# Optimization experiments

Measured on AMD Instinct MI355X. Metric: run time of the kernel, lower is better.

The kernel has to match this reference:

```python
import jax, jax.numpy as jnp
import numpy as np

LEAKY_SLOPE = 0.2

def gcn_conv(x, W, b, src, dst, deg_inv_sqrt, num_nodes):
    # GCNConv: out = D^{-1/2} (A+I) D^{-1/2} X W + b
    h = x @ W                                   # [N, out]
    norm = deg_inv_sqrt[src] * deg_inv_sqrt[dst]  # [E']
    msg = h[src] * norm[:, None]                # gather + scale
    out = jax.ops.segment_sum(msg, dst, num_segments=num_nodes)
    return out + b

def gcn_forward(x, edge_index, W1, b1, W2, b2, W3, b3):
    num_nodes = x.shape[0]
    loop = jnp.arange(num_nodes, dtype=edge_index.dtype)
    src = jnp.concatenate([edge_index[0], loop])  # add self-loops
    dst = jnp.concatenate([edge_index[1], loop])
    deg = jax.ops.segment_sum(jnp.ones_like(dst, dtype=x.dtype), dst,
                              num_segments=num_nodes)
    deg_inv_sqrt = jnp.where(deg > 0, jax.lax.rsqrt(deg), 0.0)
    # dropout is identity in eval mode (training=False)
    h = gcn_conv(x, W1, b1, src, dst, deg_inv_sqrt, num_nodes)
    h = jax.nn.leaky_relu(h, negative_slope=LEAKY_SLOPE)
    h = gcn_conv(h, W2, b2, src, dst, deg_inv_sqrt, num_nodes)
    h = jax.nn.leaky_relu(h, negative_slope=LEAKY_SLOPE)
    h = gcn_conv(h, W3, b3, src, dst, deg_inv_sqrt, num_nodes)
    return h

def setup_inputs() -> dict:
    key = jax.random.key(0)
    ks = jax.random.split(key, 8)
    N, F, E, C = 100000, 256, 3200000, 40
    x = jax.random.normal(ks[0], (N, F), dtype=jnp.float32)
    edge_index = jax.random.randint(ks[1], (2, E), 0, N, dtype=jnp.int64)
    W1 = jax.random.normal(ks[2], (F, 128), dtype=jnp.float32) * (1.0 / np.sqrt(F))
    b1 = jnp.zeros((128,), dtype=jnp.float32)
    W2 = jax.random.normal(ks[3], (128, 16), dtype=jnp.float32) * (1.0 / np.sqrt(128))
    b2 = jnp.zeros((16,), dtype=jnp.float32)
    W3 = jax.random.normal(ks[4], (16, C), dtype=jnp.float32) * (1.0 / np.sqrt(16))
    b3 = jnp.zeros((C,), dtype=jnp.float32)
    return {"x": x, "edge_index": edge_index, "W1": W1, "b1": b1,
            "W2": W2, "b2": b2, "W3": W3, "b3": b3}

def reference(x, edge_index, W1, b1, W2, b2, W3, b3):
    return gcn_forward(x, edge_index, W1, b1, W2, b2, W3, b3)
```

## Files before the change

kernel.cpp:

```cpp
#include <hip/hip_runtime.h>
#include <hip/hip_fp16.h>
#include <math.h>

#define LEAKY 0.2f
#define BP 6
#define BSZ 64
#define NBUK_MAX 2048

typedef _Float16 f16x8 __attribute__((ext_vector_type(8)));
typedef _Float16 f16x2 __attribute__((ext_vector_type(2)));
typedef float f32x4 __attribute__((ext_vector_type(4)));

union H2 { __half2 h; f16x2 f; int i; };
union H8 { __half2 h[4]; float4 f; };
union H4 { __half2 h[2]; float2 f; };

__device__ inline __half2 shfl_xor_h2(__half2 v, int m) {
    H2 u; u.h = v;
    u.i = __shfl_xor(u.i, m);
    return u.h;
}

__global__ __launch_bounds__(256) void kinit(const int* __restrict__ dst,
                                             int* __restrict__ bhist,
                                             int* __restrict__ bhB,
                                             int E, int nbuk, int chunk,
                                             const float* __restrict__ W1,
                                             __half* __restrict__ W1t,
                                             const float* __restrict__ W2,
                                             __half2* __restrict__ W2h2) {
    if (blockIdx.x < 256) {
        __shared__ int hist[NBUK_MAX];
        int t = threadIdx.x;
        for (int i = t; i < nbuk; i += 256) hist[i] = 0;
        __syncthreads();
        int base = blockIdx.x * chunk;
        int end = min(base + chunk, E);
        for (int e = base + t; e < end; e += 256)
            atomicAdd(&hist[dst[e] >> BP], 1);
        __syncthreads();
        int* myrow = bhB + (size_t)blockIdx.x * nbuk;
        for (int i = t; i < nbuk; i += 256) {
            int v = hist[i];
            myrow[i] = v;
            if (v) atomicAdd(&bhist[i], v);
        }
    } else {
        int idx = (blockIdx.x - 256) * 256 + threadIdx.x;
        if (idx < 32768) {
            int n = idx >> 8, k = idx & 255;
            W1t[idx] = __float2half(W1[k * 128 + n]);
        }
        if (idx < 1024) {
            int fp = idx >> 8;
            int r  = idx & 255;
            int e2 = r >> 6;
            int qq = (r >> 2) & 15;
            int jj = r & 3;
            float lo = W2[(qq * 8 + 2 * fp)     * 16 + e2 * 4 + jj];
            float hi = W2[(qq * 8 + 2 * fp + 1) * 16 + e2 * 4 + jj];
            W2h2[idx] = __floats2half2_rn(lo, hi);
        }
    }
}

__global__ __launch_bounds__(1024) void bscan(const int* __restrict__ bhist,
                                              int* __restrict__ bbase,
                                              int* __restrict__ bcur, int nbuk) {
    __shared__ int s[1024];
    int t = threadIdx.x;
    int v[4]; int sum = 0;
    #pragma unroll
    for (int i = 0; i < 4; ++i) {
        int idx = t * 4 + i;
        v[i] = (idx < nbuk) ? bhist[idx] : 0;
        sum += v[i];
    }
    s[t] = sum; __syncthreads();
    for (int off = 1; off < 1024; off <<= 1) {
        int a = (t >= off) ? s[t - off] : 0;
        __syncthreads();
        s[t] += a;
        __syncthreads();
    }
    int run = (t > 0) ? s[t - 1] : 0;
    #pragma unroll
    for (int i = 0; i < 4; ++i) {
        int idx = t * 4 + i;
        if (idx < nbuk) { bbase[idx] = run; bcur[idx] = run; run += v[i]; }
    }
    if (t == 1023) bbase[nbuk] = s[1023];
}

__global__ __launch_bounds__(256) void kscatter2(const int* __restrict__ src,
                                                 const int* __restrict__ dst,
                                                 int* __restrict__ bcur,
                                                 const int* __restrict__ bhB,
                                                 int* __restrict__ ebuf,
                                                 int E, int nbuk, int chunk) {
    __shared__ int hist[NBUK_MAX];
    int t = threadIdx.x;
    int base = blockIdx.x * chunk;
    int end = min(base + chunk, E);
    const int* myrow = bhB + (size_t)blockIdx.x * nbuk;
    for (int i = t; i < nbuk; i += 256) {
        int c = myrow[i];
        hist[i] = c ? atomicAdd(&bcur[i], c) : 0;
    }
    __syncthreads();
    for (int e = base + t; e < end; e += 256) {
        int d = dst[e];
        int pos = atomicAdd(&hist[d >> BP], 1);
        ebuf[pos] = ((d & (BSZ - 1)) << 17) | src[e];
    }
}

__global__ __launch_bounds__(256) void kbuild(const int* __restrict__ ebuf,
                                              const int* __restrict__ bbase,
                                              int* __restrict__ rowptr,
                                              float* __restrict__ dis,
                                              int* __restrict__ col, int N) {
    __shared__ int h[BSZ];
    __shared__ int cur[BSZ];
    int b = blockIdx.x, t = threadIdx.x;
    if (t < BSZ) h[t] = 0;
    __syncthreads();
    int beg = bbase[b], end = bbase[b + 1];
    for (int j = beg + t; j < end; j += 256)
        atomicAdd(&h[(ebuf[j] >> 17) & (BSZ - 1)], 1);
    __syncthreads();
    if (t < BSZ) {
        int node = b * BSZ + t;
        int c = (node < N) ? h[t] + 1 : 0;
        int incl = c;
        #pragma unroll
        for (int off = 1; off < 64; off <<= 1) {
            int v = __shfl_up(incl, off);
            if (t >= off) incl += v;
        }
        int colbase = beg + b * BSZ;
        if (node < N) {
            int r = colbase + incl - c;
            rowptr[node] = r;
            dis[node] = rsqrtf((float)c);
            col[r] = node;
            cur[t] = r + 1;
            if (node == N - 1) rowptr[N] = colbase + incl;
        }
    }
    __syncthreads();
    for (int j = beg + t; j < end; j += 256) {
        int v = ebuf[j];
        int p = atomicAdd(&cur[(v >> 17) & (BSZ - 1)], 1);
        col[p] = v & 0x1FFFF;
    }
}

__global__ __launch_bounds__(256) void gemm1_mfma(
        const float* __restrict__ x, const __half* __restrict__ W1t,
        const float* __restrict__ dis, __half* __restrict__ C, int M) {
    int wave = threadIdx.x >> 6;
    int lane = threadIdx.x & 63;
    int m = lane & 15, q = lane >> 4;
    int row0 = (blockIdx.x * 4 + wave) * 16;
    int arow = row0 + m;
    bool aval = arow < M;
    const float* xr = x + (size_t)arow * 256 + q * 8;
    f32x4 acc[8];
    #pragma unroll
    for (int c = 0; c < 8; ++c) acc[c] = (f32x4){0.f, 0.f, 0.f, 0.f};
    for (int k0 = 0; k0 < 256; k0 += 32) {
        f16x8 a;
        if (aval) {
            float4 v0 = *(const float4*)(xr + k0);
            float4 v1 = *(const float4*)(xr + k0 + 4);
            a[0] = (_Float16)v0.x; a[1] = (_Float16)v0.y;
            a[2] = (_Float16)v0.z; a[3] = (_Float16)v0.w;
            a[4] = (_Float16)v1.x; a[5] = (_Float16)v1.y;
            a[6] = (_Float16)v1.z; a[7] = (_Float16)v1.w;
        } else {
            #pragma unroll
            for (int i = 0; i < 8; ++i) a[i] = (_Float16)0.f;
        }
        #pragma unroll
        for (int c = 0; c < 8; ++c) {
            f16x8 b = *(const f16x8*)(W1t + (size_t)(c * 16 + m) * 256 + k0 + q * 8);
            acc[c] = __builtin_amdgcn_mfma_f32_16x16x32_f16(a, b, acc[c], 0, 0, 0);
        }
    }
    float dw[4];
    #pragma unroll
    for (int r = 0; r < 4; ++r) {
        int rr = row0 + q * 4 + r;
        dw[r] = (rr < M) ? dis[rr] : 0.f;
    }
    #pragma unroll
    for (int c = 0; c < 8; ++c) {
        #pragma unroll
        for (int r = 0; r < 4; ++r) {
            int rr = row0 + q * 4 + r;
            if (rr < M)
                C[(size_t)rr * 128 + c * 16 + m] = __float2half(acc[c][r] * dw[r]);
        }
    }
}

__global__ __launch_bounds__(256) void prop128g2(
        const __half* __restrict__ h, const int* __restrict__ rowptr,
        const int* __restrict__ col, const float* __restrict__ dis,
        const float* __restrict__ bias, const __half2* __restrict__ W2h2,
        __half* __restrict__ out, int N) {
    __shared__ __half2 swh[1024];
    {
        int k = threadIdx.x;
        ((float4*)swh)[k] = ((const float4*)W2h2)[k];
    }
    __syncthreads();

    int n = (blockIdx.x * 256 + threadIdx.x) >> 6;
    if (n >= N) return;
    int lane = threadIdx.x & 63;
    int eo = lane >> 4;
    int q = lane & 15;
    const float4* __restrict__ h4 = (const float4*)h;
    int beg = rowptr[n], end = rowptr[n + 1];
    __half2 acc[4];
    acc[0] = acc[1] = acc[2] = acc[3] = __float2half2_rn(0.f);
    int j = beg + eo;
    for (; j + 28 < end; j += 32) {
        int s0 = col[j],      s1 = col[j + 4],  s2 = col[j + 8],  s3 = col[j + 12];
        int s4 = col[j + 16], s5 = col[j + 20], s6 = col[j + 24], s7 = col[j + 28];
        H8 u0, u1, u2, u3, u4, u5, u6, u7;
        u0.f = h4[(size_t)s0 * 16 + q];
        u1.f = h4[(size_t)s1 * 16 + q];
        u2.f = h4[(size_t)s2 * 16 + q];
        u3.f = h4[(size_t)s3 * 16 + q];
        u4.f = h4[(size_t)s4 * 16 + q];
        u5.f = h4[(size_t)s5 * 16 + q];
        u6.f = h4[(size_t)s6 * 16 + q];
        u7.f = h4[(size_t)s7 * 16 + q];
        #pragma unroll
        for (int i = 0; i < 4; ++i) acc[i] = __hadd2(acc[i], u0.h[i]);
        #pragma unroll
        for (int i = 0; i < 4; ++i) acc[i] = __hadd2(acc[i], u1.h[i]);
        #pragma unroll
        for (int i = 0; i < 4; ++i) acc[i] = __hadd2(acc[i], u2.h[i]);
        #pragma unroll
        for (int i = 0; i < 4; ++i) acc[i] = __hadd2(acc[i], u3.h[i]);
        #pragma unroll
        for (int i = 0; i < 4; ++i) acc[i] = __hadd2(acc[i], u4.h[i]);
        #pragma unroll
        for (int i = 0; i < 4; ++i) acc[i] = __hadd2(acc[i], u5.h[i]);
        #pragma unroll
        for (int i = 0; i < 4; ++i) acc[i] = __hadd2(acc[i], u6.h[i]);
        #pragma unroll
        for (int i = 0; i < 4; ++i) acc[i] = __hadd2(acc[i], u7.h[i]);
    }
    for (; j + 12 < end; j += 16) {
        int s0 = col[j], s1 = col[j + 4], s2 = col[j + 8], s3 = col[j + 12];
        H8 u0, u1, u2, u3;
        u0.f = h4[(size_t)s0 * 16 + q];
        u1.f = h4[(size_t)s1 * 16 + q];
        u2.f = h4[(size_t)s2 * 16 + q];
        u3.f = h4[(size_t)s3 * 16 + q];
        #pragma unroll
        for (int i = 0; i < 4; ++i) acc[i] = __hadd2(acc[i], u0.h[i]);
        #pragma unroll
        for (int i = 0; i < 4; ++i) acc[i] = __hadd2(acc[i], u1.h[i]);
        #pragma unroll
        for (int i = 0; i < 4; ++i) acc[i] = __hadd2(acc[i], u2.h[i]);
        #pragma unroll
        for (int i = 0; i < 4; ++i) acc[i] = __hadd2(acc[i], u3.h[i]);
    }
    for (; j + 4 < end; j += 8) {
        int s0 = col[j], s1 = col[j + 4];
        H8 u0, u1;
        u0.f = h4[(size_t)s0 * 16 + q];
        u1.f = h4[(size_t)s1 * 16 + q];
        #pragma unroll
        for (int i = 0; i < 4; ++i) acc[i] = __hadd2(acc[i], u0.h[i]);
        #pragma unroll
        for (int i = 0; i < 4; ++i) acc[i] = __hadd2(acc[i], u1.h[i]);
    }
    for (; j < end; j += 4) {
        int s = col[j];
        H8 u; u.f = h4[(size_t)s * 16 + q];
        #pragma unroll
        for (int i = 0; i < 4; ++i) acc[i] = __hadd2(acc[i], u.h[i]);
    }
    #pragma unroll
    for (int i = 0; i < 4; ++i) {
        acc[i] = __hadd2(acc[i], shfl_xor_h2(acc[i], 16));
        acc[i] = __hadd2(acc[i], shfl_xor_h2(acc[i], 32));
    }
    float dn = dis[n];
    const float4* b4 = (const float4*)bias;
    float4 bA = b4[q * 2];
    float4 bB = b4[q * 2 + 1];
    float2 f0 = __half22float2(acc[0]);
    float2 f1 = __half22float2(acc[1]);
    float2 f2 = __half22float2(acc[2]);
    float2 f3 = __half22float2(acc[3]);
    float xf[8];
    xf[0] = fmaf(dn, f0.x, bA.x); xf[1] = fmaf(dn, f0.y, bA.y);
    xf[2] = fmaf(dn, f1.x, bA.z); xf[3] = fmaf(dn, f1.y, bA.w);
    xf[4] = fmaf(dn, f2.x, bB.x); xf[5] = fmaf(dn, f2.y, bB.y);
    xf[6] = fmaf(dn, f3.x, bB.z); xf[7] = fmaf(dn, f3.y, bB.w);
    #pragma unroll
    for (int i = 0; i < 8; ++i) xf[i] = xf[i] > 0.f ? xf[i] : LEAKY * xf[i];
    H2 xh[4];
    #pragma unroll
    for (int fp = 0; fp < 4; ++fp)
        xh[fp].h = __floats2half2_rn(xf[2 * fp], xf[2 * fp + 1]);
    float p0 = 0.f, p1 = 0.f, p2 = 0.f, p3 = 0.f;
    #pragma unroll
    for (int fp = 0; fp < 4; ++fp) {
        H8 wv;
        wv.f = *(const float4*)&swh[fp * 256 + eo * 64 + q * 4];
        H2 w0, w1, w2, w3;
        w0.h = wv.h[0]; w1.h = wv.h[1]; w2.h = wv.h[2]; w3.h = wv.h[3];
        p0 = __builtin_amdgcn_fdot2(xh[fp].f, w0.f, p0, false);
        p1 = __builtin_amdgcn_fdot2(xh[fp].f, w1.f, p1, false);
        p2 = __builtin_amdgcn_fdot2(xh[fp].f, w2.f, p2, false);
        p3 = __builtin_amdgcn_fdot2(xh[fp].f, w3.f, p3, false);
    }
    #pragma unroll
    for (int mm = 1; mm < 16; mm <<= 1) {
        p0 += __shfl_xor(p0, mm);
        p1 += __shfl_xor(p1, mm);
        p2 += __shfl_xor(p2, mm);
        p3 += __shfl_xor(p3, mm);
    }
    if (q == 0) {
        H4 w;
        w.h[0] = __floats2half2_rn(p0 * dn, p1 * dn);
        w.h[1] = __floats2half2_rn(p2 * dn, p3 * dn);
        ((float2*)out)[(size_t)n * 4 + eo] = w.f;
    }
}

__global__ __launch_bounds__(256) void prop16(
        const __half* __restrict__ h, const int* __restrict__ rowptr,
        const int* __restrict__ col, const float* __restrict__ dis,
        const float* __restrict__ bias, __half* __restrict__ outp, int N) {
    int t = blockIdx.x * 256 + threadIdx.x;
    int n = t >> 3;
    if (n >= N) return;
    int li = threadIdx.x & 7;
    int slot = li >> 1;
    int half = li & 1;
    const float4* __restrict__ h4 = (const float4*)h;
    int beg = rowptr[n], end = rowptr[n + 1];
    __half2 acc[4];
    acc[0] = acc[1] = acc[2] = acc[3] = __float2half2_rn(0.f);
    int j = beg + slot;
    for (; j + 12 < end; j += 16) {
        int s0 = col[j], s1 = col[j + 4], s2 = col[j + 8], s3 = col[j + 12];
        H8 u0, u1, u2, u3;
        u0.f = h4[(size_t)s0 * 2 + half];
        u1.f = h4[(size_t)s1 * 2 + half];
        u2.f = h4[(size_t)s2 * 2 + half];
        u3.f = h4[(size_t)s3 * 2 + half];
        #pragma unroll
        for (int i = 0; i < 4; ++i) acc[i] = __hadd2(acc[i], u0.h[i]);
        #pragma unroll
        for (int i = 0; i < 4; ++i) acc[i] = __hadd2(acc[i], u1.h[i]);
        #pragma unroll
        for (int i = 0; i < 4; ++i) acc[i] = __hadd2(acc[i], u2.h[i]);
        #pragma unroll
        for (int i = 0; i < 4; ++i) acc[i] = __hadd2(acc[i], u3.h[i]);
    }
    for (; j + 4 < end; j += 8) {
        int s0 = col[j], s1 = col[j + 4];
        H8 u0, u1;
        u0.f = h4[(size_t)s0 * 2 + half];
        u1.f = h4[(size_t)s1 * 2 + half];
        #pragma unroll
        for (int i = 0; i < 4; ++i) acc[i] = __hadd2(acc[i], u0.h[i]);
        #pragma unroll
        for (int i = 0; i < 4; ++i) acc[i] = __hadd2(acc[i], u1.h[i]);
    }
    for (; j < end; j += 4) {
        int s = col[j];
        H8 u; u.f = h4[(size_t)s * 2 + half];
        #pragma unroll
        for (int i = 0; i < 4; ++i) acc[i] = __hadd2(acc[i], u.h[i]);
    }
    #pragma unroll
    for (int i = 0; i < 4; ++i) {
        acc[i] = __hadd2(acc[i], shfl_xor_h2(acc[i], 2));
        acc[i] = __hadd2(acc[i], shfl_xor_h2(acc[i], 4));
    }
    if (slot == 0) {
        float dn = dis[n];
        const float4* b4 = (const float4*)bias;
        float4 bA = b4[half * 2];
        float4 bB = b4[half * 2 + 1];
        float2 f0 = __half22float2(acc[0]);
        float2 f1 = __half22float2(acc[1]);
        float2 f2 = __half22float2(acc[2]);
        float2 f3 = __half22float2(acc[3]);
        float o0 = fmaf(dn, f0.x, bA.x), o1 = fmaf(dn, f0.y, bA.y);
        float o2 = fmaf(dn, f1.x, bA.z), o3 = fmaf(dn, f1.y, bA.w);
        float o4 = fmaf(dn, f2.x, bB.x), o5 = fmaf(dn, f2.y, bB.y);
        float o6 = fmaf(dn, f3.x, bB.z), o7 = fmaf(dn, f3.y, bB.w);
        o0 = o0 > 0.f ? o0 : LEAKY * o0;  o1 = o1 > 0.f ? o1 : LEAKY * o1;
        o2 = o2 > 0.f ? o2 : LEAKY * o2;  o3 = o3 > 0.f ? o3 : LEAKY * o3;
        o4 = o4 > 0.f ? o4 : LEAKY * o4;  o5 = o5 > 0.f ? o5 : LEAKY * o5;
        o6 = o6 > 0.f ? o6 : LEAKY * o6;  o7 = o7 > 0.f ? o7 : LEAKY * o7;
        o0 *= dn; o1 *= dn; o2 *= dn; o3 *= dn;
        o4 *= dn; o5 *= dn; o6 *= dn; o7 *= dn;
        H8 w;
        w.h[0] = __floats2half2_rn(o0, o1);
        w.h[1] = __floats2half2_rn(o2, o3);
        w.h[2] = __floats2half2_rn(o4, o5);
        w.h[3] = __floats2half2_rn(o6, o7);
        ((float4*)outp)[(size_t)n * 2 + half] = w.f;
    }
}

__global__ __launch_bounds__(256) void prop16_gemm3(
        const __half* __restrict__ h, const int* __restrict__ rowptr,
        const int* __restrict__ col, const float* __restrict__ dis,
        const float* __restrict__ W3, const float* __restrict__ b3,
        float* __restrict__ out, int N) {
    __shared__ float sw[640];
    __shared__ float sb[40];
    int t0 = threadIdx.x;
    for (int i = t0; i < 640; i += 256) sw[i] = W3[i];
    if (t0 < 40) sb[t0] = b3[t0];
    __syncthreads();
    int t = blockIdx.x * 256 + t0;
    int n = t >> 3;
    if (n >= N) return;
    int li = t0 & 7;
    int slot = li >> 1;
    int half = li & 1;
    const float4* __restrict__ h4 = (const float4*)h;
    int beg = rowptr[n], end = rowptr[n + 1];
    __half2 acc[4];
    acc[0] = acc[1] = acc[2] = acc[3] = __float2half2_rn(0.f);
    int j = beg + slot;
    for (; j + 12 < end; j += 16) {
        int s0 = col[j], s1 = col[j + 4], s2 = col[j + 8], s3 = col[j + 12];
        H8 u0, u1, u2, u3;
        u0.f = h4[(size_t)s0 * 2 + half];
        u1.f = h4[(size_t)s1 * 2 + half];
        u2.f = h4[(size_t)s2 * 2 + half];
        u3.f = h4[(size_t)s3 * 2 + half];
        #pragma unroll
        for (int i = 0; i < 4; ++i) acc[i] = __hadd2(acc[i], u0.h[i]);
        #pragma unroll
        for (int i = 0; i < 4; ++i) acc[i] = __hadd2(acc[i], u1.h[i]);
        #pragma unroll
        for (int i = 0; i < 4; ++i) acc[i] = __hadd2(acc[i], u2.h[i]);
        #pragma unroll
        for (int i = 0; i < 4; ++i) acc[i] = __hadd2(acc[i], u3.h[i]);
    }
    for (; j + 4 < end; j += 8) {
        int s0 = col[j], s1 = col[j + 4];
        H8 u0, u1;
        u0.f = h4[(size_t)s0 * 2 + half];
        u1.f = h4[(size_t)s1 * 2 + half];
        #pragma unroll
        for (int i = 0; i < 4; ++i) acc[i] = __hadd2(acc[i], u0.h[i]);
        #pragma unroll
        for (int i = 0; i < 4; ++i) acc[i] = __hadd2(acc[i], u1.h[i]);
    }
    for (; j < end; j += 4) {
        int s = col[j];
        H8 u; u.f = h4[(size_t)s * 2 + half];
        #pragma unroll
        for (int i = 0; i < 4; ++i) acc[i] = __hadd2(acc[i], u.h[i]);
    }
    #pragma unroll
    for (int i = 0; i < 4; ++i) {
        acc[i] = __hadd2(acc[i], shfl_xor_h2(acc[i], 2));
        acc[i] = __hadd2(acc[i], shfl_xor_h2(acc[i], 4));
    }
    __half2 oth[4];
    #pragma unroll
    for (int i = 0; i < 4; ++i) oth[i] = shfl_xor_h2(acc[i], 1);
    float dn = dis[n];
    float p[16];
    #pragma unroll
    for (int i = 0; i < 4; ++i) {
        __half2 lo = half ? oth[i] : acc[i];
        __half2 hi = half ? acc[i] : oth[i];
        float2 a = __half22float2(lo);
        float2 b = __half22float2(hi);
        p[2 * i]     = dn * a.x;  p[2 * i + 1]     = dn * a.y;
        p[8 + 2 * i] = dn * b.x;  p[8 + 2 * i + 1] = dn * b.y;
    }
    float o0 = 0.f, o1 = 0.f, o2 = 0.f, o3 = 0.f, o4 = 0.f;
    #pragma unroll
    for (int k = 0; k < 16; ++k) {
        const float* wr = &sw[k * 40 + li];
        o0 = fmaf(p[k], wr[0],  o0);
        o1 = fmaf(p[k], wr[8],  o1);
        o2 = fmaf(p[k], wr[16], o2);
        o3 = fmaf(p[k], wr[24], o3);
        o4 = fmaf(p[k], wr[32], o4);
    }
    float* orow = out + (size_t)n * 40;
    orow[li]      = o0 + sb[li];
    orow[li + 8]  = o1 + sb[li + 8];
    orow[li + 16] = o2 + sb[li + 16];
    orow[li + 24] = o3 + sb[li + 24];
    orow[li + 32] = o4 + sb[li + 32];
}


extern "C" void kernel_launch(void* const* d_in, const int* in_sizes, int n_in,
                              void* d_out, int out_size, void* d_ws, size_t ws_size,
                              hipStream_t stream) {
    const float* x  = (const float*)d_in[0];
    const int*   ei = (const int*)d_in[1];
    const float* W1 = (const float*)d_in[2];
    const float* b1 = (const float*)d_in[3];
    const float* W2 = (const float*)d_in[4];
    const float* b2 = (const float*)d_in[5];
    const float* W3 = (const float*)d_in[6];
    const float* b3 = (const float*)d_in[7];
    float* out = (float*)d_out;

    int N = in_sizes[0] / 256;
    int E = in_sizes[1] / 2;
    const int* src = ei;
    const int* dst = ei + E;
    int NBUK = (N + BSZ - 1) >> BP;

    char* w = (char*)d_ws;
    auto alloc = [&](size_t bytes) {
        char* p = w;
        w += (bytes + 255) & ~(size_t)255;
        return p;
    };
    int*     rowptr  = (int*)    alloc((size_t)(N + 1) * 4);
    int*     bhist   = (int*)    alloc((size_t)NBUK * 4);
    int*     bbase   = (int*)    alloc((size_t)(NBUK + 1) * 4);
    int*     bcur    = (int*)    alloc((size_t)NBUK * 4);
    int*     bhB     = (int*)    alloc((size_t)256 * NBUK * 4);
    int*     ebuf    = (int*)    alloc((size_t)E * 4);
    int*     colx    = (int*)    alloc((size_t)(E + N) * 4);
    float*   dis     = (float*)  alloc((size_t)N * 4);
    __half*  W1t     = (__half*) alloc((size_t)128 * 256 * 2);
    __half2* W2h2    = (__half2*)alloc((size_t)1024 * 4);
    __half*  h1h     = (__half*) alloc((size_t)N * 128 * 2);
    __half*  h2h     = (__half*) alloc((size_t)N * 16 * 2);
    __half*  x2h     = (__half*) alloc((size_t)N * 16 * 2);

    int SC_BLOCKS = 256;
    int chunk = (E + SC_BLOCKS - 1) / SC_BLOCKS;

    (void)hipMemsetAsync(bhist, 0, (size_t)NBUK * 4, stream);
    kinit   <<<384, 256, 0, stream>>>(dst, bhist, bhB, E, NBUK, chunk,
                                      W1, W1t, W2, W2h2);
    bscan   <<<1, 1024, 0, stream>>>(bhist, bbase, bcur, NBUK);
    kscatter2<<<SC_BLOCKS, 256, 0, stream>>>(src, dst, bcur, bhB, ebuf, E, NBUK, chunk);
    kbuild  <<<NBUK, 256, 0, stream>>>(ebuf, bbase, rowptr, dis, colx, N);

    int gtiles = (N + 63) / 64;
    gemm1_mfma<<<gtiles, 256, 0, stream>>>(x, W1t, dis, h1h, N);
    prop128g2 <<<(N * 64 + 255) / 256, 256, 0, stream>>>(h1h, rowptr, colx,
                                                         dis, b1, W2h2, h2h, N);
    prop16    <<<(N * 8 + 255) / 256, 256, 0, stream>>>(h2h, rowptr, colx,
                                                        dis, b2, x2h, N);
    prop16_gemm3<<<(N * 8 + 255) / 256, 256, 0, stream>>>(x2h, rowptr, colx,
                                                          dis, W3, b3, out, N);
}
```

Measured before the change: 509.7 us.

## Build CSR with per-node global atomics instead of bucketed two-pass sort

Replaces the bucket histogram, bucket scatter into a temporary edge buffer, and per-bucket CSR build with a direct per-node degree count via global atomics, a block-sum plus scan for row offsets, and a direct scatter of sources into column slots using per-node atomic cursors. This removes the intermediate edge buffer and one pass over the edges. In exchange it relies on millions of global-memory atomics, whose throughput and contention may cost more than the shared-memory atomics they replace.

New measurement: 677.5 us. 1.33x slower.

```diff
diff --git a/kernel.cpp b/kernel.cpp
--- a/kernel.cpp
+++ b/kernel.cpp
@@ -3,9 +3,7 @@
 #include <math.h>
 
 #define LEAKY 0.2f
-#define BP 6
 #define BSZ 64
-#define NBUK_MAX 2048
 
 typedef _Float16 f16x8 __attribute__((ext_vector_type(8)));
 typedef _Float16 f16x2 __attribute__((ext_vector_type(2)));
@@ -22,29 +20,18 @@
 }
 
 __global__ __launch_bounds__(256) void kinit(const int* __restrict__ dst,
-                                             int* __restrict__ bhist,
-                                             int* __restrict__ bhB,
-                                             int E, int nbuk, int chunk,
+                                             int* __restrict__ ncnt,
+                                             int E, int chunk,
                                              const float* __restrict__ W1,
                                              __half* __restrict__ W1t,
                                              const float* __restrict__ W2,
                                              __half2* __restrict__ W2h2) {
     if (blockIdx.x < 256) {
-        __shared__ int hist[NBUK_MAX];
         int t = threadIdx.x;
-        for (int i = t; i < nbuk; i += 256) hist[i] = 0;
-        __syncthreads();
         int base = blockIdx.x * chunk;
         int end = min(base + chunk, E);
         for (int e = base + t; e < end; e += 256)
-            atomicAdd(&hist[dst[e] >> BP], 1);
-        __syncthreads();
-        int* myrow = bhB + (size_t)blockIdx.x * nbuk;
-        for (int i = t; i < nbuk; i += 256) {
-            int v = hist[i];
-            myrow[i] = v;
-            if (v) atomicAdd(&bhist[i], v);
-        }
+            atomicAdd(&ncnt[dst[e]], 1);
     } else {
         int idx = (blockIdx.x - 256) * 256 + threadIdx.x;
         if (idx < 32768) {
@@ -64,9 +51,17 @@
     }
 }
 
+__global__ __launch_bounds__(64) void bsum(const int* __restrict__ ncnt,
+                                           int* __restrict__ bhist, int N) {
+    int node = blockIdx.x * 64 + threadIdx.x;
+    int c = (node < N) ? ncnt[node] : 0;
+    #pragma unroll
+    for (int off = 32; off; off >>= 1) c += __shfl_down(c, off);
+    if (threadIdx.x == 0) bhist[blockIdx.x] = c;
+}
+
 __global__ __launch_bounds__(1024) void bscan(const int* __restrict__ bhist,
-                                              int* __restrict__ bbase,
-                                              int* __restrict__ bcur, int nbuk) {
+                                              int* __restrict__ bbase, int nbuk) {
     __shared__ int s[1024];
     int t = threadIdx.x;
     int v[4]; int sum = 0;
@@ -87,72 +82,47 @@
     #pragma unroll
     for (int i = 0; i < 4; ++i) {
         int idx = t * 4 + i;
-        if (idx < nbuk) { bbase[idx] = run; bcur[idx] = run; run += v[i]; }
+        if (idx < nbuk) { bbase[idx] = run; run += v[i]; }
     }
     if (t == 1023) bbase[nbuk] = s[1023];
 }
 
-__global__ __launch_bounds__(256) void kscatter2(const int* __restrict__ src,
-                                                 const int* __restrict__ dst,
-                                                 int* __restrict__ bcur,
-                                                 const int* __restrict__ bhB,
-                                                 int* __restrict__ ebuf,
-                                                 int E, int nbuk, int chunk) {
-    __shared__ int hist[NBUK_MAX];
+__global__ __launch_bounds__(64) void kplace2(const int* __restrict__ ncnt,
+                                              const int* __restrict__ bbase,
+                                              int* __restrict__ rowptr,
+                                              float* __restrict__ dis,
+                                              int* __restrict__ col,
+                                              int* __restrict__ gcur, int N) {
+    int b = blockIdx.x, t = threadIdx.x;
+    int node = b * 64 + t;
+    int c = (node < N) ? ncnt[node] + 1 : 0;
+    int incl = c;
+    #pragma unroll
+    for (int off = 1; off < 64; off <<= 1) {
+        int v = __shfl_up(incl, off);
+        if (t >= off) incl += v;
+    }
+    int colbase = bbase[b] + b * 64;
+    if (node < N) {
+        int r = colbase + incl - c;
+        rowptr[node] = r;
+        dis[node] = rsqrtf((float)c);
+        col[r] = node;
+        gcur[node] = r + 1;
+        if (node == N - 1) rowptr[N] = colbase + incl;
+    }
+}
+
+__global__ __launch_bounds__(256) void kscatter_direct(
+        const int* __restrict__ src, const int* __restrict__ dst,
+        int* __restrict__ gcur, int* __restrict__ col, int E, int chunk) {
     int t = threadIdx.x;
     int base = blockIdx.x * chunk;
     int end = min(base + chunk, E);
-    const int* myrow = bhB + (size_t)blockIdx.x * nbuk;
-    for (int i = t; i < nbuk; i += 256) {
-        int c = myrow[i];
-        hist[i] = c ? atomicAdd(&bcur[i], c) : 0;
-    }
-    __syncthreads();
     for (int e = base + t; e < end; e += 256) {
         int d = dst[e];
-        int pos = atomicAdd(&hist[d >> BP], 1);
-        ebuf[pos] = ((d & (BSZ - 1)) << 17) | src[e];
-    }
-}
-
-__global__ __launch_bounds__(256) void kbuild(const int* __restrict__ ebuf,
-                                              const int* __restrict__ bbase,
-                                              int* __restrict__ rowptr,
-                                              float* __restrict__ dis,
-                                              int* __restrict__ col, int N) {
-    __shared__ int h[BSZ];
-    __shared__ int cur[BSZ];
-    int b = blockIdx.x, t = threadIdx.x;
-    if (t < BSZ) h[t] = 0;
-    __syncthreads();
-    int beg = bbase[b], end = bbase[b + 1];
-    for (int j = beg + t; j < end; j += 256)
-        atomicAdd(&h[(ebuf[j] >> 17) & (BSZ - 1)], 1);
-    __syncthreads();
-    if (t < BSZ) {
-        int node = b * BSZ + t;
-        int c = (node < N) ? h[t] + 1 : 0;
-        int incl = c;
-        #pragma unroll
-        for (int off = 1; off < 64; off <<= 1) {
-            int v = __shfl_up(incl, off);
-            if (t >= off) incl += v;
-        }
-        int colbase = beg + b * BSZ;
-        if (node < N) {
-            int r = colbase + incl - c;
-            rowptr[node] = r;
-            dis[node] = rsqrtf((float)c);
-            col[r] = node;
-            cur[t] = r + 1;
-            if (node == N - 1) rowptr[N] = colbase + incl;
-        }
-    }
-    __syncthreads();
-    for (int j = beg + t; j < end; j += 256) {
-        int v = ebuf[j];
-        int p = atomicAdd(&cur[(v >> 17) & (BSZ - 1)], 1);
-        col[p] = v & 0x1FFFF;
+        int p = atomicAdd(&gcur[d], 1);
+        col[p] = src[e];
     }
 }
 
@@ -528,7 +498,7 @@
     int E = in_sizes[1] / 2;
     const int* src = ei;
     const int* dst = ei + E;
-    int NBUK = (N + BSZ - 1) >> BP;
+    int NBUK = (N + BSZ - 1) / BSZ;
 
     char* w = (char*)d_ws;
     auto alloc = [&](size_t bytes) {
@@ -539,9 +509,8 @@
     int*     rowptr  = (int*)    alloc((size_t)(N + 1) * 4);
     int*     bhist   = (int*)    alloc((size_t)NBUK * 4);
     int*     bbase   = (int*)    alloc((size_t)(NBUK + 1) * 4);
-    int*     bcur    = (int*)    alloc((size_t)NBUK * 4);
-    int*     bhB     = (int*)    alloc((size_t)256 * NBUK * 4);
-    int*     ebuf    = (int*)    alloc((size_t)E * 4);
+    int*     ncnt    = (int*)    alloc((size_t)N * 4);
+    int*     gcur    = (int*)    alloc((size_t)N * 4);
     int*     colx    = (int*)    alloc((size_t)(E + N) * 4);
     float*   dis     = (float*)  alloc((size_t)N * 4);
     __half*  W1t     = (__half*) alloc((size_t)128 * 256 * 2);
@@ -553,12 +522,12 @@
     int SC_BLOCKS = 256;
     int chunk = (E + SC_BLOCKS - 1) / SC_BLOCKS;
 
-    (void)hipMemsetAsync(bhist, 0, (size_t)NBUK * 4, stream);
-    kinit   <<<384, 256, 0, stream>>>(dst, bhist, bhB, E, NBUK, chunk,
-                                      W1, W1t, W2, W2h2);
-    bscan   <<<1, 1024, 0, stream>>>(bhist, bbase, bcur, NBUK);
-    kscatter2<<<SC_BLOCKS, 256, 0, stream>>>(src, dst, bcur, bhB, ebuf, E, NBUK, chunk);
-    kbuild  <<<NBUK, 256, 0, stream>>>(ebuf, bbase, rowptr, dis, colx, N);
+    (void)hipMemsetAsync(ncnt, 0, (size_t)N * 4, stream);
+    kinit   <<<384, 256, 0, stream>>>(dst, ncnt, E, chunk, W1, W1t, W2, W2h2);
+    bsum    <<<NBUK, 64, 0, stream>>>(ncnt, bhist, N);
+    bscan   <<<1, 1024, 0, stream>>>(bhist, bbase, NBUK);
+    kplace2 <<<NBUK, 64, 0, stream>>>(ncnt, bbase, rowptr, dis, colx, gcur, N);
+    kscatter_direct<<<SC_BLOCKS, 256, 0, stream>>>(src, dst, gcur, colx, E, chunk);
 
     int gtiles = (N + 63) / 64;
     gemm1_mfma<<<gtiles, 256, 0, stream>>>(x, W1t, dis, h1h, N);
```
